# Optimization experiments

Measured on AMD Instinct MI355X. Metric: run time of the kernel, lower is better.

The kernel has to match this reference:

```python
import jax, jax.numpy as jnp
import numpy as np

N_ATOMS = 100000
N_MOLS = 5000
IN_F = 1008
H1, H2, H3 = 256, 192, 160
OUT_C = 1
ELEMS = np.array([1, 6, 7, 8, 9])  # H, C, N, O, F
ALPHA = 0.1


def setup_inputs() -> dict:
    key = jax.random.key(0)
    ks = jax.random.split(key, 12)
    zidx = jax.random.randint(ks[0], (N_ATOMS,), 0, 5)
    z = jnp.asarray(ELEMS)[zidx].astype(jnp.int64)
    features = jax.random.normal(ks[1], (N_ATOMS, IN_F), dtype=jnp.float32)
    batch = jnp.sort(jax.random.randint(ks[2], (N_ATOMS,), 0, N_MOLS)).astype(jnp.int64)
    # Stacked per-element MLP params: leading axis = 5 element types (H,C,N,O,F)
    def w(k, shape, fan_in):
        return jax.random.normal(k, shape, dtype=jnp.float32) / np.sqrt(fan_in)
    W1 = w(ks[3], (5, IN_F, H1), IN_F); b1 = jnp.zeros((5, H1), jnp.float32)
    W2 = w(ks[4], (5, H1, H2), H1);     b2 = jnp.zeros((5, H2), jnp.float32)
    W3 = w(ks[5], (5, H2, H3), H2);     b3 = jnp.zeros((5, H3), jnp.float32)
    W4 = w(ks[6], (5, H3, OUT_C), H3);  b4 = jnp.zeros((5, OUT_C), jnp.float32)
    return {"z": z, "features": features, "batch": batch, "n_mols": N_MOLS,
            "W1": W1, "b1": b1, "W2": W2, "b2": b2,
            "W3": W3, "b3": b3, "W4": W4, "b4": b4}


def _celu(x):
    return jax.nn.celu(x, alpha=ALPHA)


def reference(z, features, batch, n_mols, W1, b1, W2, b2, W3, b3, W4, b4):
    # Per-element-type MLPs run over all atoms (t = 5 element types), then the
    # atom's true type is selected via a one-hot mask -- equivalent to the
    # gather -> per-type MLP -> scatter-back in the torch forward.
    h = _celu(jnp.einsum('nf,tfh->tnh', features, W1) + b1[:, None, :])
    h = _celu(jnp.einsum('tnh,thg->tng', h, W2) + b2[:, None, :])
    h = _celu(jnp.einsum('tng,tgk->tnk', h, W3) + b3[:, None, :])
    v_all = jnp.einsum('tnk,tko->tno', h, W4) + b4[:, None, :]  # [5, N, out]
    onehot = (z[None, :] == jnp.asarray(ELEMS)[:, None]).astype(features.dtype)  # [5, N]
    v = jnp.einsum('tn,tno->no', onehot, v_all)  # [N, out]
    u = jax.ops.segment_sum(v, batch, num_segments=n_mols)  # [n_mols, out]
    return u
```

## Files before the change

### kernel.cpp

```cpp
#include <hip/hip_runtime.h>
#include <stdint.h>

#define NF    1008
#define KP1   1024
#define NH1   256
#define NH2   192
#define NH3   160
#define MT    64
#define CELU_ALPHA 0.1f

typedef __attribute__((ext_vector_type(8))) __bf16 bf16x8;
typedef __attribute__((ext_vector_type(4))) float  f32x4;

#define W1T_OFF   0u
#define W2T_OFF   2621440u
#define W3T_OFF   3112960u
#define META_OFF  3420160u
#define SORT_OFF  3420288u

__device__ __forceinline__ unsigned short f2bf(float f) {
  union { float f; uint32_t u; } v; v.f = f;
  uint32_t u = v.u;
  uint32_t r = u + 0x7FFFu + ((u >> 16) & 1u);
  return (unsigned short)(r >> 16);
}

__device__ __forceinline__ float celu_f(float x) {
  return x > 0.f ? x : CELU_ALPHA * (__expf(x * (1.f / CELU_ALPHA)) - 1.f);
}

__device__ __forceinline__ int ztype(int z) {
  return z == 1 ? 0 : z == 6 ? 1 : z == 7 ? 2 : z == 8 ? 3 : 4;
}


__global__ void prep_weights(const float* __restrict__ W1, const float* __restrict__ W2,
                             const float* __restrict__ W3,
                             unsigned short* __restrict__ w1t, unsigned short* __restrict__ w2t,
                             unsigned short* __restrict__ w3t) {
  int bid = blockIdx.x;
  const float* src; unsigned short* dst; int K, N, KP, kt, nt;
  if (bid < 320) {
    int t = bid / 64, r = bid % 64; kt = r / 4; nt = r % 4;
    src = W1 + (size_t)t * NF * NH1; dst = w1t + (size_t)t * NH1 * KP1;
    K = NF; N = NH1; KP = KP1;
  } else if (bid < 380) {
    int b = bid - 320; int t = b / 12, r = b % 12; kt = r / 3; nt = r % 3;
    src = W2 + (size_t)t * NH1 * NH2; dst = w2t + (size_t)t * NH2 * NH1;
    K = NH1; N = NH2; KP = NH1;
  } else {
    int b = bid - 380; int t = b / 9, r = b % 9; kt = r / 3; nt = r % 3;
    src = W3 + (size_t)t * NH2 * NH3; dst = w3t + (size_t)t * NH3 * NH2;
    K = NH2; N = NH3; KP = NH2;
  }
  __shared__ float tile[64][65];
  int k0 = kt * 64, n0 = nt * 64;
  int tid = threadIdx.x;
  {
    int nl = tid & 63, kb = tid >> 6;
    #pragma unroll
    for (int i = 0; i < 16; ++i) {
      int kl = kb + 4 * i;
      int k = k0 + kl, n = n0 + nl;
      tile[kl][nl] = (k < K && n < N) ? src[(size_t)k * N + n] : 0.f;
    }
  }
  __syncthreads();
  {
    int klw = tid & 63, nb = tid >> 6;
    #pragma unroll
    for (int i = 0; i < 16; ++i) {
      int nl = nb + 4 * i;
      int n = n0 + nl, k = k0 + klw;
      if (n < N && k < KP) dst[(size_t)n * KP + k] = f2bf(tile[klw][nl]);
    }
  }
}

__global__ void hist_types(const int* __restrict__ z, int n, int* __restrict__ counts) {
  __shared__ int h[5];
  if (threadIdx.x < 5) h[threadIdx.x] = 0;
  __syncthreads();
  int i = blockIdx.x * blockDim.x + threadIdx.x;
  if (i < n) atomicAdd(&h[ztype(z[i])], 1);
  __syncthreads();
  if (threadIdx.x < 5 && h[threadIdx.x]) atomicAdd(&counts[threadIdx.x], h[threadIdx.x]);
}

__global__ void plan_tiles(const int* __restrict__ counts, int* __restrict__ atom_base,
                           int* __restrict__ tile_base) {
  if (threadIdx.x == 0 && blockIdx.x == 0) {
    int a = 0, tb = 0;
    for (int t = 0; t < 5; ++t) {
      atom_base[t] = a; tile_base[t] = tb;
      a += counts[t]; tb += (counts[t] + MT - 1) / MT;
    }
    atom_base[5] = a; tile_base[5] = tb;
  }
}

__global__ void scatter_atoms(const int* __restrict__ z, int n,
                              const int* __restrict__ atom_base, int* __restrict__ cursors,
                              int* __restrict__ sorted) {
  int i = blockIdx.x * blockDim.x + threadIdx.x;
  int lane = threadIdx.x & 63;
  int t = (i < n) ? ztype(z[i]) : -1;
  #pragma unroll
  for (int tt = 0; tt < 5; ++tt) {
    unsigned long long mask = __ballot(t == tt);
    if (t == tt) {
      int leader = __ffsll((long long)mask) - 1;
      int rank = __popcll(mask & ((1ull << lane) - 1ull));
      int base = 0;
      if (lane == leader) base = atomicAdd(&cursors[tt], (int)__popcll(mask));
      base = __shfl(base, leader);
      sorted[atom_base[tt] + base + rank] = i;
    }
  }
}

__global__ __launch_bounds__(256, 2) void fcnn_main(
    const float* __restrict__ feat, const int* __restrict__ batch,
    const unsigned short* __restrict__ w1t, const unsigned short* __restrict__ w2t,
    const unsigned short* __restrict__ w3t, const float* __restrict__ W4,
    const float* __restrict__ b1, const float* __restrict__ b2,
    const float* __restrict__ b3, const float* __restrict__ b4,
    const int* __restrict__ atom_base, const int* __restrict__ tile_base,
    const int* __restrict__ sorted_idx, float* __restrict__ out) {
  __shared__ __align__(16) unsigned char smem[59648];
  unsigned short* Abuf = (unsigned short*)smem;
  unsigned short* h2s  = (unsigned short*)smem;
  unsigned short* h1s  = (unsigned short*)(smem + 25600);
  unsigned short* h3s  = (unsigned short*)(smem + 25600);
  int* lgid = (int*)(smem + 59392);

  const int bid = blockIdx.x;
  if (bid >= tile_base[5]) return;
  int t = 0;
  #pragma unroll
  for (int i = 0; i < 4; ++i) if (bid >= tile_base[i + 1]) t = i + 1;
  const int m0 = atom_base[t] + (bid - tile_base[t]) * MT;
  const int rows = min(MT, atom_base[t + 1] - m0);

  const int tid = threadIdx.x;
  const int lane = tid & 63;
  const int w = tid >> 6;
  const int col = lane & 15;
  const int q = lane >> 4;

  if (tid < MT) lgid[tid] = (tid < rows) ? sorted_idx[m0 + tid] : -1;
  __syncthreads();

  const int srow = tid >> 2;
  const int sc4 = tid & 3;
  const int sg = lgid[srow];
  const float* fsrc = (sg >= 0) ? (feat + (size_t)sg * NF) : feat;
  const unsigned short* w1p = w1t + (size_t)t * NH1 * KP1;

  f32x4 acc[4][4];
  #pragma unroll
  for (int a = 0; a < 4; ++a)
    #pragma unroll
    for (int b = 0; b < 4; ++b) acc[a][b] = (f32x4){0.f, 0.f, 0.f, 0.f};

  f32x4 sv[4];
  #pragma unroll
  for (int i = 0; i < 4; ++i) {
    int c = sc4 + 4 * i;
    int k = c * 4;
    sv[i] = (sg >= 0 && k < NF) ? *(const f32x4*)(fsrc + k) : (f32x4){0.f, 0.f, 0.f, 0.f};
  }
  {
    unsigned short* dst = Abuf;
    #pragma unroll
    for (int i = 0; i < 4; ++i) {
      int c = sc4 + 4 * i;
      ushort4 pk;
      pk.x = f2bf(sv[i][0]); pk.y = f2bf(sv[i][1]); pk.z = f2bf(sv[i][2]); pk.w = f2bf(sv[i][3]);
      *(ushort4*)(dst + srow * 72 + c * 4) = pk;
    }
  }
  __syncthreads();

  #pragma unroll 1
  for (int kc = 0; kc < 16; ++kc) {
    const int cur = kc & 1;
    f32x4 nv[4];
    if (kc < 15) {
      #pragma unroll
      for (int i = 0; i < 4; ++i) {
        int c = sc4 + 4 * i;
        int k = (kc + 1) * 64 + c * 4;
        nv[i] = (sg >= 0 && k < NF) ? *(const f32x4*)(fsrc + k) : (f32x4){0.f, 0.f, 0.f, 0.f};
      }
    }
    const unsigned short* ab = Abuf + cur * 4608;
    #pragma unroll
    for (int ks = 0; ks < 2; ++ks) {
      bf16x8 af[4];
      #pragma unroll
      for (int im = 0; im < 4; ++im)
        af[im] = *(const bf16x8*)(ab + (im * 16 + col) * 72 + ks * 32 + q * 8);
      #pragma unroll
      for (int jj = 0; jj < 4; ++jj) {
        int n = (w + 4 * jj) * 16 + col;
        bf16x8 bfr = *(const bf16x8*)(w1p + (size_t)n * KP1 + kc * 64 + ks * 32 + q * 8);
        #pragma unroll
        for (int im = 0; im < 4; ++im)
          acc[im][jj] = __builtin_amdgcn_mfma_f32_16x16x32_bf16(af[im], bfr, acc[im][jj], 0, 0, 0);
      }
    }
    if (kc < 15) {
      unsigned short* dst = Abuf + (cur ^ 1) * 4608;
      #pragma unroll
      for (int i = 0; i < 4; ++i) {
        int c = sc4 + 4 * i;
        ushort4 pk;
        pk.x = f2bf(nv[i][0]); pk.y = f2bf(nv[i][1]); pk.z = f2bf(nv[i][2]); pk.w = f2bf(nv[i][3]);
        *(ushort4*)(dst + srow * 72 + c * 4) = pk;
      }
    }
    __syncthreads();
  }

  #pragma unroll
  for (int jj = 0; jj < 4; ++jj) {
    int n = (w + 4 * jj) * 16 + col;
    float bias = b1[t * NH1 + n];
    #pragma unroll
    for (int im = 0; im < 4; ++im)
      #pragma unroll
      for (int r = 0; r < 4; ++r)
        h1s[(im * 16 + q * 4 + r) * 264 + n] = f2bf(celu_f(acc[im][jj][r] + bias));
  }
  __syncthreads();

  f32x4 acc2[4][3];
  #pragma unroll
  for (int a = 0; a < 4; ++a)
    #pragma unroll
    for (int b = 0; b < 3; ++b) acc2[a][b] = (f32x4){0.f, 0.f, 0.f, 0.f};
  const unsigned short* w2p = w2t + (size_t)t * NH2 * NH1;
  #pragma unroll
  for (int ks = 0; ks < 8; ++ks) {
    bf16x8 af[4];
    #pragma unroll
    for (int im = 0; im < 4; ++im)
      af[im] = *(const bf16x8*)(h1s + (im * 16 + col) * 264 + ks * 32 + q * 8);
    #pragma unroll
    for (int jj = 0; jj < 3; ++jj) {
      int n = (w + 4 * jj) * 16 + col;
      bf16x8 bfr = *(const bf16x8*)(w2p + (size_t)n * NH1 + ks * 32 + q * 8);
      #pragma unroll
      for (int im = 0; im < 4; ++im)
        acc2[im][jj] = __builtin_amdgcn_mfma_f32_16x16x32_bf16(af[im], bfr, acc2[im][jj], 0, 0, 0);
    }
  }
  #pragma unroll
  for (int jj = 0; jj < 3; ++jj) {
    int n = (w + 4 * jj) * 16 + col;
    float bias = b2[t * NH2 + n];
    #pragma unroll
    for (int im = 0; im < 4; ++im)
      #pragma unroll
      for (int r = 0; r < 4; ++r)
        h2s[(im * 16 + q * 4 + r) * 200 + n] = f2bf(celu_f(acc2[im][jj][r] + bias));
  }
  __syncthreads();

  f32x4 acc3[4][3];
  #pragma unroll
  for (int a = 0; a < 4; ++a)
    #pragma unroll
    for (int b = 0; b < 3; ++b) acc3[a][b] = (f32x4){0.f, 0.f, 0.f, 0.f};
  const unsigned short* w3p = w3t + (size_t)t * NH3 * NH2;
  #pragma unroll
  for (int ks = 0; ks < 6; ++ks) {
    bf16x8 af[4];
    #pragma unroll
    for (int im = 0; im < 4; ++im)
      af[im] = *(const bf16x8*)(h2s + (im * 16 + col) * 200 + ks * 32 + q * 8);
    #pragma unroll
    for (int jj = 0; jj < 3; ++jj) {
      int j = w + 4 * jj;
      if (j < 10) {
        int n = j * 16 + col;
        bf16x8 bfr = *(const bf16x8*)(w3p + (size_t)n * NH2 + ks * 32 + q * 8);
        #pragma unroll
        for (int im = 0; im < 4; ++im)
          acc3[im][jj] = __builtin_amdgcn_mfma_f32_16x16x32_bf16(af[im], bfr, acc3[im][jj], 0, 0, 0);
      }
    }
  }
  #pragma unroll
  for (int jj = 0; jj < 3; ++jj) {
    int j = w + 4 * jj;
    if (j < 10) {
      int n = j * 16 + col;
      float bias = b3[t * NH3 + n];
      #pragma unroll
      for (int im = 0; im < 4; ++im)
        #pragma unroll
        for (int r = 0; r < 4; ++r)
          h3s[(im * 16 + q * 4 + r) * 168 + n] = f2bf(celu_f(acc3[im][jj][r] + bias));
    }
  }
  __syncthreads();

  {
    int a = tid >> 2, p = tid & 3;
    float v = 0.f;
    if (a < rows) {
      const float* wp = W4 + t * NH3;
      #pragma unroll
      for (int c0 = 0; c0 < 5; ++c0) {
        int c = p + 4 * c0;
        bf16x8 hv = *(const bf16x8*)(h3s + a * 168 + c * 8);
        #pragma unroll
        for (int j = 0; j < 8; ++j) v += (float)hv[j] * wp[c * 8 + j];
      }
    }
    v += __shfl_xor(v, 1);
    v += __shfl_xor(v, 2);
    if (p == 0 && a < rows) {
      int g = lgid[a];
      atomicAdd(&out[batch[g]], v + b4[t]);
    }
  }
}

extern "C" void kernel_launch(void* const* d_in, const int* in_sizes, int n_in,
                              void* d_out, int out_size, void* d_ws, size_t ws_size,
                              hipStream_t stream) {
  const int*   z    = (const int*)d_in[0];
  const float* feat = (const float*)d_in[1];
  const int*   bat  = (const int*)d_in[2];
  const float* W1 = (const float*)d_in[4];
  const float* b1 = (const float*)d_in[5];
  const float* W2 = (const float*)d_in[6];
  const float* b2 = (const float*)d_in[7];
  const float* W3 = (const float*)d_in[8];
  const float* b3 = (const float*)d_in[9];
  const float* W4 = (const float*)d_in[10];
  const float* b4 = (const float*)d_in[11];
  const int n = in_sizes[0];

  unsigned char* ws = (unsigned char*)d_ws;
  unsigned short* w1t = (unsigned short*)(ws + W1T_OFF);
  unsigned short* w2t = (unsigned short*)(ws + W2T_OFF);
  unsigned short* w3t = (unsigned short*)(ws + W3T_OFF);
  int* meta = (int*)(ws + META_OFF);
  int* counts    = meta;
  int* atom_base = meta + 8;
  int* tile_base = meta + 16;
  int* cursors   = meta + 24;
  int* sorted    = (int*)(ws + SORT_OFF);

  hipMemsetAsync(meta, 0, 128, stream);
  hipMemsetAsync(d_out, 0, (size_t)out_size * sizeof(float), stream);

  prep_weights<<<425, 256, 0, stream>>>(W1, W2, W3, w1t, w2t, w3t);
  int nb = (n + 255) / 256;
  hist_types<<<nb, 256, 0, stream>>>(z, n, counts);
  plan_tiles<<<1, 64, 0, stream>>>(counts, atom_base, tile_base);
  scatter_atoms<<<nb, 256, 0, stream>>>(z, n, atom_base, cursors, sorted);
  int max_tiles = n / MT + 6;
  fcnn_main<<<max_tiles, 256, 0, stream>>>(feat, bat, w1t, w2t, w3t, W4,
                                           b1, b2, b3, b4,
                                           atom_base, tile_base, sorted,
                                           (float*)d_out);
  (void)n_in; (void)ws_size;
}
```

Before: 803.2 us.

## Use 512-thread blocks with 256-wide K chunks and fuse weight prep with histogram

```diff
diff --git a/kernel.cpp b/kernel.cpp
--- a/kernel.cpp
+++ b/kernel.cpp
@@ -33,12 +33,23 @@
   return z == 1 ? 0 : z == 6 ? 1 : z == 7 ? 2 : z == 8 ? 3 : 4;
 }
 
-
-__global__ void prep_weights(const float* __restrict__ W1, const float* __restrict__ W2,
-                             const float* __restrict__ W3,
-                             unsigned short* __restrict__ w1t, unsigned short* __restrict__ w2t,
-                             unsigned short* __restrict__ w3t) {
+__global__ void prep_and_hist(const float* __restrict__ W1, const float* __restrict__ W2,
+                              const float* __restrict__ W3,
+                              unsigned short* __restrict__ w1t, unsigned short* __restrict__ w2t,
+                              unsigned short* __restrict__ w3t,
+                              const int* __restrict__ z, int n, int* __restrict__ counts) {
   int bid = blockIdx.x;
+  int tid = threadIdx.x;
+  if (bid >= 425) {
+    __shared__ int h[5];
+    if (tid < 5) h[tid] = 0;
+    __syncthreads();
+    int i = (bid - 425) * 256 + tid;
+    if (i < n) atomicAdd(&h[ztype(z[i])], 1);
+    __syncthreads();
+    if (tid < 5 && h[tid]) atomicAdd(&counts[tid], h[tid]);
+    return;
+  }
   const float* src; unsigned short* dst; int K, N, KP, kt, nt;
   if (bid < 320) {
     int t = bid / 64, r = bid % 64; kt = r / 4; nt = r % 4;
@@ -55,36 +66,25 @@
   }
   __shared__ float tile[64][65];
   int k0 = kt * 64, n0 = nt * 64;
-  int tid = threadIdx.x;
   {
     int nl = tid & 63, kb = tid >> 6;
     #pragma unroll
     for (int i = 0; i < 16; ++i) {
       int kl = kb + 4 * i;
-      int k = k0 + kl, n = n0 + nl;
-      tile[kl][nl] = (k < K && n < N) ? src[(size_t)k * N + n] : 0.f;
+      int k = k0 + kl, nn = n0 + nl;
+      tile[kl][nl] = (k < K && nn < N) ? src[(size_t)k * N + nn] : 0.f;
     }
   }
   __syncthreads();
   {
-    int klw = tid & 63, nb = tid >> 6;
+    int klw = tid & 63, nb2 = tid >> 6;
     #pragma unroll
     for (int i = 0; i < 16; ++i) {
-      int nl = nb + 4 * i;
-      int n = n0 + nl, k = k0 + klw;
-      if (n < N && k < KP) dst[(size_t)n * KP + k] = f2bf(tile[klw][nl]);
-    }
-  }
-}
-
-__global__ void hist_types(const int* __restrict__ z, int n, int* __restrict__ counts) {
-  __shared__ int h[5];
-  if (threadIdx.x < 5) h[threadIdx.x] = 0;
-  __syncthreads();
-  int i = blockIdx.x * blockDim.x + threadIdx.x;
-  if (i < n) atomicAdd(&h[ztype(z[i])], 1);
-  __syncthreads();
-  if (threadIdx.x < 5 && h[threadIdx.x]) atomicAdd(&counts[threadIdx.x], h[threadIdx.x]);
+      int nl = nb2 + 4 * i;
+      int nn = n0 + nl, k = k0 + klw;
+      if (nn < N && k < KP) dst[(size_t)nn * KP + k] = f2bf(tile[klw][nl]);
+    }
+  }
 }
 
 __global__ void plan_tiles(const int* __restrict__ counts, int* __restrict__ atom_base,
@@ -119,7 +119,7 @@
   }
 }
 
-__global__ __launch_bounds__(256, 2) void fcnn_main(
+__global__ __launch_bounds__(512, 4) void fcnn_main(
     const float* __restrict__ feat, const int* __restrict__ batch,
     const unsigned short* __restrict__ w1t, const unsigned short* __restrict__ w2t,
     const unsigned short* __restrict__ w3t, const float* __restrict__ W4,
@@ -127,12 +127,13 @@
     const float* __restrict__ b3, const float* __restrict__ b4,
     const int* __restrict__ atom_base, const int* __restrict__ tile_base,
     const int* __restrict__ sorted_idx, float* __restrict__ out) {
-  __shared__ __align__(16) unsigned char smem[59648];
-  unsigned short* Abuf = (unsigned short*)smem;
-  unsigned short* h2s  = (unsigned short*)smem;
-  unsigned short* h1s  = (unsigned short*)(smem + 25600);
-  unsigned short* h3s  = (unsigned short*)(smem + 25600);
-  int* lgid = (int*)(smem + 59392);
+  __shared__ __align__(16) unsigned char smem[67840];
+  unsigned short* A0  = (unsigned short*)smem;
+  unsigned short* A1  = (unsigned short*)(smem + 33792);
+  unsigned short* h1s = (unsigned short*)smem;
+  unsigned short* h2s = (unsigned short*)(smem + 33792);
+  unsigned short* h3s = (unsigned short*)smem;
+  int* lgid = (int*)(smem + 67584);
 
   const int bid = blockIdx.x;
   if (bid >= tile_base[5]) return;
@@ -151,81 +152,74 @@
   if (tid < MT) lgid[tid] = (tid < rows) ? sorted_idx[m0 + tid] : -1;
   __syncthreads();
 
-  const int srow = tid >> 2;
-  const int sc4 = tid & 3;
+  const int srow = tid >> 3;
+  const int sl = tid & 7;
   const int sg = lgid[srow];
   const float* fsrc = (sg >= 0) ? (feat + (size_t)sg * NF) : feat;
   const unsigned short* w1p = w1t + (size_t)t * NH1 * KP1;
 
-  f32x4 acc[4][4];
+  f32x4 acc[4][2];
   #pragma unroll
   for (int a = 0; a < 4; ++a)
     #pragma unroll
-    for (int b = 0; b < 4; ++b) acc[a][b] = (f32x4){0.f, 0.f, 0.f, 0.f};
-
-  f32x4 sv[4];
-  #pragma unroll
-  for (int i = 0; i < 4; ++i) {
-    int c = sc4 + 4 * i;
-    int k = c * 4;
-    sv[i] = (sg >= 0 && k < NF) ? *(const f32x4*)(fsrc + k) : (f32x4){0.f, 0.f, 0.f, 0.f};
-  }
-  {
-    unsigned short* dst = Abuf;
-    #pragma unroll
-    for (int i = 0; i < 4; ++i) {
-      int c = sc4 + 4 * i;
-      ushort4 pk;
-      pk.x = f2bf(sv[i][0]); pk.y = f2bf(sv[i][1]); pk.z = f2bf(sv[i][2]); pk.w = f2bf(sv[i][3]);
-      *(ushort4*)(dst + srow * 72 + c * 4) = pk;
-    }
+    for (int b = 0; b < 2; ++b) acc[a][b] = (f32x4){0.f, 0.f, 0.f, 0.f};
+
+  f32x4 nv[8];
+  #pragma unroll
+  for (int i = 0; i < 8; ++i) {
+    int k = (sl + 8 * i) * 4;
+    nv[i] = (sg >= 0 && k < NF) ? *(const f32x4*)(fsrc + k) : (f32x4){0.f, 0.f, 0.f, 0.f};
+  }
+  #pragma unroll
+  for (int i = 0; i < 8; ++i) {
+    int c = sl + 8 * i;
+    ushort4 pk;
+    pk.x = f2bf(nv[i][0]); pk.y = f2bf(nv[i][1]); pk.z = f2bf(nv[i][2]); pk.w = f2bf(nv[i][3]);
+    *(ushort4*)(A0 + srow * 264 + c * 4) = pk;
   }
   __syncthreads();
 
   #pragma unroll 1
-  for (int kc = 0; kc < 16; ++kc) {
-    const int cur = kc & 1;
-    f32x4 nv[4];
-    if (kc < 15) {
-      #pragma unroll
-      for (int i = 0; i < 4; ++i) {
-        int c = sc4 + 4 * i;
-        int k = (kc + 1) * 64 + c * 4;
+  for (int kc = 0; kc < 4; ++kc) {
+    if (kc < 3) {
+      #pragma unroll
+      for (int i = 0; i < 8; ++i) {
+        int k = (kc + 1) * 256 + (sl + 8 * i) * 4;
         nv[i] = (sg >= 0 && k < NF) ? *(const f32x4*)(fsrc + k) : (f32x4){0.f, 0.f, 0.f, 0.f};
       }
     }
-    const unsigned short* ab = Abuf + cur * 4608;
-    #pragma unroll
-    for (int ks = 0; ks < 2; ++ks) {
+    const unsigned short* ab = (kc & 1) ? A1 : A0;
+    #pragma unroll
+    for (int ks = 0; ks < 8; ++ks) {
       bf16x8 af[4];
       #pragma unroll
       for (int im = 0; im < 4; ++im)
-        af[im] = *(const bf16x8*)(ab + (im * 16 + col) * 72 + ks * 32 + q * 8);
-      #pragma unroll
-      for (int jj = 0; jj < 4; ++jj) {
-        int n = (w + 4 * jj) * 16 + col;
-        bf16x8 bfr = *(const bf16x8*)(w1p + (size_t)n * KP1 + kc * 64 + ks * 32 + q * 8);
+        af[im] = *(const bf16x8*)(ab + (im * 16 + col) * 264 + ks * 32 + q * 8);
+      #pragma unroll
+      for (int jj = 0; jj < 2; ++jj) {
+        int n = (w + 8 * jj) * 16 + col;
+        bf16x8 bfr = *(const bf16x8*)(w1p + (size_t)n * KP1 + kc * 256 + ks * 32 + q * 8);
         #pragma unroll
         for (int im = 0; im < 4; ++im)
           acc[im][jj] = __builtin_amdgcn_mfma_f32_16x16x32_bf16(af[im], bfr, acc[im][jj], 0, 0, 0);
       }
     }
-    if (kc < 15) {
-      unsigned short* dst = Abuf + (cur ^ 1) * 4608;
-      #pragma unroll
-      for (int i = 0; i < 4; ++i) {
-        int c = sc4 + 4 * i;
+    if (kc < 3) {
+      unsigned short* dst = (kc & 1) ? A0 : A1;
+      #pragma unroll
+      for (int i = 0; i < 8; ++i) {
+        int c = sl + 8 * i;
         ushort4 pk;
         pk.x = f2bf(nv[i][0]); pk.y = f2bf(nv[i][1]); pk.z = f2bf(nv[i][2]); pk.w = f2bf(nv[i][3]);
-        *(ushort4*)(dst + srow * 72 + c * 4) = pk;
+        *(ushort4*)(dst + srow * 264 + c * 4) = pk;
       }
     }
     __syncthreads();
   }
 
   #pragma unroll
-  for (int jj = 0; jj < 4; ++jj) {
-    int n = (w + 4 * jj) * 16 + col;
+  for (int jj = 0; jj < 2; ++jj) {
+    int n = (w + 8 * jj) * 16 + col;
     float bias = b1[t * NH1 + n];
     #pragma unroll
     for (int im = 0; im < 4; ++im)
@@ -235,11 +229,11 @@
   }
   __syncthreads();
 
-  f32x4 acc2[4][3];
+  f32x4 acc2[4][2];
   #pragma unroll
   for (int a = 0; a < 4; ++a)
     #pragma unroll
-    for (int b = 0; b < 3; ++b) acc2[a][b] = (f32x4){0.f, 0.f, 0.f, 0.f};
+    for (int b = 0; b < 2; ++b) acc2[a][b] = (f32x4){0.f, 0.f, 0.f, 0.f};
   const unsigned short* w2p = w2t + (size_t)t * NH2 * NH1;
   #pragma unroll
   for (int ks = 0; ks < 8; ++ks) {
@@ -248,31 +242,37 @@
     for (int im = 0; im < 4; ++im)
       af[im] = *(const bf16x8*)(h1s + (im * 16 + col) * 264 + ks * 32 + q * 8);
     #pragma unroll
-    for (int jj = 0; jj < 3; ++jj) {
-      int n = (w + 4 * jj) * 16 + col;
-      bf16x8 bfr = *(const bf16x8*)(w2p + (size_t)n * NH1 + ks * 32 + q * 8);
+    for (int jj = 0; jj < 2; ++jj) {
+      int j = w + 8 * jj;
+      if (j < 12) {
+        int n = j * 16 + col;
+        bf16x8 bfr = *(const bf16x8*)(w2p + (size_t)n * NH1 + ks * 32 + q * 8);
+        #pragma unroll
+        for (int im = 0; im < 4; ++im)
+          acc2[im][jj] = __builtin_amdgcn_mfma_f32_16x16x32_bf16(af[im], bfr, acc2[im][jj], 0, 0, 0);
+      }
+    }
+  }
+  #pragma unroll
+  for (int jj = 0; jj < 2; ++jj) {
+    int j = w + 8 * jj;
+    if (j < 12) {
+      int n = j * 16 + col;
+      float bias = b2[t * NH2 + n];
       #pragma unroll
       for (int im = 0; im < 4; ++im)
-        acc2[im][jj] = __builtin_amdgcn_mfma_f32_16x16x32_bf16(af[im], bfr, acc2[im][jj], 0, 0, 0);
-    }
-  }
-  #pragma unroll
-  for (int jj = 0; jj < 3; ++jj) {
-    int n = (w + 4 * jj) * 16 + col;
-    float bias = b2[t * NH2 + n];
-    #pragma unroll
-    for (int im = 0; im < 4; ++im)
-      #pragma unroll
-      for (int r = 0; r < 4; ++r)
-        h2s[(im * 16 + q * 4 + r) * 200 + n] = f2bf(celu_f(acc2[im][jj][r] + bias));
-  }
-  __syncthreads();
-
-  f32x4 acc3[4][3];
+        #pragma unroll
+        for (int r = 0; r < 4; ++r)
+          h2s[(im * 16 + q * 4 + r) * 200 + n] = f2bf(celu_f(acc2[im][jj][r] + bias));
+    }
+  }
+  __syncthreads();
+
+  f32x4 acc3[4][2];
   #pragma unroll
   for (int a = 0; a < 4; ++a)
     #pragma unroll
-    for (int b = 0; b < 3; ++b) acc3[a][b] = (f32x4){0.f, 0.f, 0.f, 0.f};
+    for (int b = 0; b < 2; ++b) acc3[a][b] = (f32x4){0.f, 0.f, 0.f, 0.f};
   const unsigned short* w3p = w3t + (size_t)t * NH3 * NH2;
   #pragma unroll
   for (int ks = 0; ks < 6; ++ks) {
@@ -281,8 +281,8 @@
     for (int im = 0; im < 4; ++im)
       af[im] = *(const bf16x8*)(h2s + (im * 16 + col) * 200 + ks * 32 + q * 8);
     #pragma unroll
-    for (int jj = 0; jj < 3; ++jj) {
-      int j = w + 4 * jj;
+    for (int jj = 0; jj < 2; ++jj) {
+      int j = w + 8 * jj;
       if (j < 10) {
         int n = j * 16 + col;
         bf16x8 bfr = *(const bf16x8*)(w3p + (size_t)n * NH2 + ks * 32 + q * 8);
@@ -293,8 +293,8 @@
     }
   }
   #pragma unroll
-  for (int jj = 0; jj < 3; ++jj) {
-    int j = w + 4 * jj;
+  for (int jj = 0; jj < 2; ++jj) {
+    int j = w + 8 * jj;
     if (j < 10) {
       int n = j * 16 + col;
       float bias = b3[t * NH3 + n];
@@ -308,20 +308,23 @@
   __syncthreads();
 
   {
-    int a = tid >> 2, p = tid & 3;
+    int a = tid >> 3, p = tid & 7;
     float v = 0.f;
     if (a < rows) {
       const float* wp = W4 + t * NH3;
       #pragma unroll
-      for (int c0 = 0; c0 < 5; ++c0) {
-        int c = p + 4 * c0;
-        bf16x8 hv = *(const bf16x8*)(h3s + a * 168 + c * 8);
-        #pragma unroll
-        for (int j = 0; j < 8; ++j) v += (float)hv[j] * wp[c * 8 + j];
+      for (int c0 = 0; c0 < 3; ++c0) {
+        int c = p + 8 * c0;
+        if (c < 20) {
+          bf16x8 hv = *(const bf16x8*)(h3s + a * 168 + c * 8);
+          #pragma unroll
+          for (int j = 0; j < 8; ++j) v += (float)hv[j] * wp[c * 8 + j];
+        }
       }
     }
     v += __shfl_xor(v, 1);
     v += __shfl_xor(v, 2);
+    v += __shfl_xor(v, 4);
     if (p == 0 && a < rows) {
       int g = lgid[a];
       atomicAdd(&out[batch[g]], v + b4[t]);
@@ -359,13 +362,12 @@
   hipMemsetAsync(meta, 0, 128, stream);
   hipMemsetAsync(d_out, 0, (size_t)out_size * sizeof(float), stream);
 
-  prep_weights<<<425, 256, 0, stream>>>(W1, W2, W3, w1t, w2t, w3t);
   int nb = (n + 255) / 256;
-  hist_types<<<nb, 256, 0, stream>>>(z, n, counts);
+  prep_and_hist<<<425 + nb, 256, 0, stream>>>(W1, W2, W3, w1t, w2t, w3t, z, n, counts);
   plan_tiles<<<1, 64, 0, stream>>>(counts, atom_base, tile_base);
   scatter_atoms<<<nb, 256, 0, stream>>>(z, n, atom_base, cursors, sorted);
   int max_tiles = n / MT + 6;
-  fcnn_main<<<max_tiles, 256, 0, stream>>>(feat, bat, w1t, w2t, w3t, W4,
+  fcnn_main<<<max_tiles, 512, 0, stream>>>(feat, bat, w1t, w2t, w3t, W4,
                                            b1, b2, b3, b4,
                                            atom_base, tile_base, sorted,
                                            (float*)d_out);
```

Result: faster. 783.8 us (-2.4%).
